# Performance work log

Hardware: AMD Instinct MI355X
Metric: run time of the kernel (lower is better)

## Reference

```python
import jax, jax.numpy as jnp
import numpy as np

def setup_inputs() -> dict:
    key = jax.random.key(0)
    k1, k2, k3 = jax.random.split(key, 3)
    B, N, D = 4, 2048, 1024
    x = jax.random.normal(k1, (B, N, D), dtype=jnp.float32)
    # nn.Linear weights are (out_features, in_features); init scale ~1/sqrt(D)
    W_Q = jax.random.normal(k2, (D, D), dtype=jnp.float32) / np.sqrt(D)
    W_K = jax.random.normal(k3, (D, D), dtype=jnp.float32) / np.sqrt(D)
    return {"x": x, "W_Q": W_Q, "W_K": W_K, "n_iters": 5}

def reference(x, W_Q, W_K, n_iters):
    # K = Linear(W_K)(x) = x @ W_K.T  -> (B, N, D)
    K = jnp.einsum('bnd,kd->bnk', x, W_K)
    y = x
    for _ in range(n_iters):
        Q = jnp.einsum('bnd,kd->bnk', y, W_Q)          # (B, N, D)
        scores = jnp.einsum('bnd,bmd->bnm', K, Q)       # K @ Q^T, (B, N, N)
        probs = jax.nn.softmax(scores, axis=-1)
        y = jnp.einsum('bnm,bmd->bnd', probs, x)        # (B, N, D)
    return y
```

## Files before the change

### kernel.cpp

```cpp
#include <hip/hip_runtime.h>
#include <cstdint>

typedef _Float16 f16;
typedef __attribute__((ext_vector_type(8))) _Float16 v8h;
typedef __attribute__((ext_vector_type(4))) float v4f;

#define LO_SCALE 4096.0f
#define LO_INV   2.44140625e-4f

__device__ __forceinline__ void split2(float f, f16& h, f16& l) {
    h = (f16)f;
    l = (f16)((f - (float)h) * LO_SCALE);
}

__device__ __forceinline__ void gload_lds16(const void* g, void* l) {
    __builtin_amdgcn_global_load_lds(
        (const __attribute__((address_space(1))) unsigned int*)(uintptr_t)g,
        (__attribute__((address_space(3))) unsigned int*)(unsigned int)(uintptr_t)l,
        16, 0, 0);
}

__global__ __launch_bounds__(256)
void gemm_nt_2limb(const f16* __restrict__ A1, const f16* __restrict__ A2,
                   const f16* __restrict__ B1, const f16* __restrict__ B2,
                   float* __restrict__ C32, f16* __restrict__ Ch,
                   f16* __restrict__ Cl, int mode, int N, int K)
{
    __shared__ f16 lds[4 * 128 * 32];
    f16* lA1 = lds;
    f16* lA2 = lds + 128 * 32;
    f16* lB1 = lds + 2 * 128 * 32;
    f16* lB2 = lds + 3 * 128 * 32;

    const int tid  = threadIdx.x;
    const int lane = tid & 63;
    const int wave = tid >> 6;
    const int wm = wave >> 1, wn = wave & 1;
    const int fr = lane & 15, quad = lane >> 4;
    const int row0 = blockIdx.y * 128;
    const int col0 = blockIdx.x * 128;
    const int l4 = lane >> 2;
    const int c8 = (lane & 3) * 8;

    v4f accB[4][4], accS[4][4];
#pragma unroll
    for (int i = 0; i < 4; ++i)
#pragma unroll
        for (int j = 0; j < 4; ++j) {
            accB[i][j] = {0.f, 0.f, 0.f, 0.f};
            accS[i][j] = {0.f, 0.f, 0.f, 0.f};
        }

    for (int k0 = 0; k0 < K; k0 += 32) {
#pragma unroll
        for (int t = 0; t < 2; ++t) {
            const int slot = wave + 4 * t;
            const int r = slot * 16 + l4;
            const size_t ga = (size_t)(row0 + r) * K + (k0 + c8);
            const size_t gb = (size_t)(col0 + r) * K + (k0 + c8);
            const unsigned loff = slot * 1024;
            gload_lds16(A1 + ga, (char*)lA1 + loff);
            gload_lds16(A2 + ga, (char*)lA2 + loff);
            gload_lds16(B1 + gb, (char*)lB1 + loff);
            gload_lds16(B2 + gb, (char*)lB2 + loff);
        }
        __syncthreads();

        v8h a1[4], a2[4], b1[4], b2[4];
#pragma unroll
        for (int i = 0; i < 4; ++i) {
            const int off = (wm * 64 + i * 16 + fr) * 32 + quad * 8;
            a1[i] = *(const v8h*)&lA1[off];
            a2[i] = *(const v8h*)&lA2[off];
        }
#pragma unroll
        for (int j = 0; j < 4; ++j) {
            const int off = (wn * 64 + j * 16 + fr) * 32 + quad * 8;
            b1[j] = *(const v8h*)&lB1[off];
            b2[j] = *(const v8h*)&lB2[off];
        }
#pragma unroll
        for (int i = 0; i < 4; ++i)
#pragma unroll
            for (int j = 0; j < 4; ++j) {
                accB[i][j] = __builtin_amdgcn_mfma_f32_16x16x32_f16(a1[i], b1[j], accB[i][j], 0, 0, 0);
                accS[i][j] = __builtin_amdgcn_mfma_f32_16x16x32_f16(a2[i], b1[j], accS[i][j], 0, 0, 0);
                accS[i][j] = __builtin_amdgcn_mfma_f32_16x16x32_f16(a1[i], b2[j], accS[i][j], 0, 0, 0);
            }
        __syncthreads();
    }

#pragma unroll
    for (int i = 0; i < 4; ++i)
#pragma unroll
        for (int j = 0; j < 4; ++j) {
            const int row = row0 + wm * 64 + i * 16 + quad * 4;
            const int col = col0 + wn * 64 + j * 16 + fr;
#pragma unroll
            for (int r = 0; r < 4; ++r) {
                const float v = accB[i][j][r] + accS[i][j][r] * LO_INV;
                const size_t off = (size_t)(row + r) * N + col;
                if (mode == 0) {
                    C32[off] = v;
                } else if (mode == 1) {
                    f16 h, l; split2(v, h, l);
                    Ch[off] = h; Cl[off] = l;
                } else {
                    C32[off] = v;
                    Ch[off] = (f16)v;
                }
            }
        }
}

__global__ __launch_bounds__(512)
void gemm_nt_2limb_256(const f16* __restrict__ A1, const f16* __restrict__ A2,
                       const f16* __restrict__ B1, const f16* __restrict__ B2,
                       float* __restrict__ C32, f16* __restrict__ Ch,
                       int N, int K)
{
    __shared__ f16 lds[2 * 24576];

    const int bid = blockIdx.x;
    const int lid = (bid & 7) * 32 + (bid >> 3);
    const int col0 = (lid & 7) * 128;
    const int row0 = (lid >> 3) * 256;

    const int tid  = threadIdx.x;
    const int lane = tid & 63;
    const int wave = tid >> 6;
    const int wm = wave >> 1;
    const int wn = wave & 1;
    const int fr = lane & 15, quad = lane >> 4;
    const int NT = K >> 5;

    const int trow = tid >> 2;
    const int tchunk = tid & 3;

    auto STAGE = [&](int T) {
        const unsigned bufB = (unsigned)(T & 1) * 49152u;
        const int k0 = T * 32;
#pragma unroll
        for (int rd = 0; rd < 2; ++rd) {
            const int r = trow + rd * 128;
            const int sc = (tchunk ^ ((r >> 1) & 3)) * 8;
            const size_t ga = (size_t)(row0 + r) * K + k0 + sc;
            const unsigned dof = (unsigned)(rd * 8192 + wave * 1024);
            gload_lds16(A1 + ga, (char*)lds + bufB + dof);
            gload_lds16(A2 + ga, (char*)lds + bufB + 16384u + dof);
        }
        {
            const int r = trow;
            const int sc = (tchunk ^ ((r >> 1) & 3)) * 8;
            const size_t gb = (size_t)(col0 + r) * K + k0 + sc;
            const unsigned dof = (unsigned)(wave * 1024);
            gload_lds16(B1 + gb, (char*)lds + bufB + 32768u + dof);
            gload_lds16(B2 + gb, (char*)lds + bufB + 40960u + dof);
        }
    };

    auto LRD = [&](const f16* base, int row) {
        return *(const v8h*)&base[row * 32 + ((quad ^ ((row >> 1) & 3)) * 8)];
    };

    v4f accB[4][4], accS[4][4];
#pragma unroll
    for (int i = 0; i < 4; ++i)
#pragma unroll
        for (int j = 0; j < 4; ++j) {
            accB[i][j] = {0.f, 0.f, 0.f, 0.f};
            accS[i][j] = {0.f, 0.f, 0.f, 0.f};
        }

    STAGE(0);
    asm volatile("s_waitcnt vmcnt(0)" ::: "memory");
    __builtin_amdgcn_s_barrier();

    for (int t = 0; t < NT; ++t) {
        const int bc = (t & 1) * 24576;
        const f16* lA1 = lds + bc;
        const f16* lA2 = lds + bc + 8192;
        const f16* lB1 = lds + bc + 16384;
        const f16* lB2 = lds + bc + 20480;

        v8h b1[4], b2[4];
#pragma unroll
        for (int j = 0; j < 4; ++j) {
            b1[j] = LRD(lB1, wn * 64 + j * 16 + fr);
            b2[j] = LRD(lB2, wn * 64 + j * 16 + fr);
        }
        {
            v8h a1 = LRD(lA1, wm * 64 + 0 + fr);
            v8h a2 = LRD(lA2, wm * 64 + 0 + fr);
            if (t + 1 < NT) STAGE(t + 1);
            __builtin_amdgcn_s_barrier();
            asm volatile("s_waitcnt lgkmcnt(0)" ::: "memory");
            __builtin_amdgcn_s_setprio(1);
#pragma unroll
            for (int j = 0; j < 4; ++j) {
                accB[0][j] = __builtin_amdgcn_mfma_f32_16x16x32_f16(a1, b1[j], accB[0][j], 0, 0, 0);
                accS[0][j] = __builtin_amdgcn_mfma_f32_16x16x32_f16(a2, b1[j], accS[0][j], 0, 0, 0);
                accS[0][j] = __builtin_amdgcn_mfma_f32_16x16x32_f16(a1, b2[j], accS[0][j], 0, 0, 0);
            }
            __builtin_amdgcn_s_setprio(0);
            __builtin_amdgcn_s_barrier();
        }

#pragma unroll
        for (int p = 1; p < 4; ++p) {
            v8h a1 = LRD(lA1, wm * 64 + p * 16 + fr);
            v8h a2 = LRD(lA2, wm * 64 + p * 16 + fr);
            __builtin_amdgcn_s_barrier();
            asm volatile("s_waitcnt lgkmcnt(0)" ::: "memory");
            __builtin_amdgcn_s_setprio(1);
#pragma unroll
            for (int j = 0; j < 4; ++j) {
                accB[p][j] = __builtin_amdgcn_mfma_f32_16x16x32_f16(a1, b1[j], accB[p][j], 0, 0, 0);
                accS[p][j] = __builtin_amdgcn_mfma_f32_16x16x32_f16(a2, b1[j], accS[p][j], 0, 0, 0);
                accS[p][j] = __builtin_amdgcn_mfma_f32_16x16x32_f16(a1, b2[j], accS[p][j], 0, 0, 0);
            }
            __builtin_amdgcn_s_setprio(0);
            if (p == 3)
                asm volatile("s_waitcnt vmcnt(0)" ::: "memory");
            __builtin_amdgcn_s_barrier();
        }
    }

#pragma unroll
    for (int i = 0; i < 4; ++i)
#pragma unroll
        for (int j = 0; j < 4; ++j) {
            const int row = row0 + wm * 64 + i * 16 + quad * 4;
            const int col = col0 + wn * 64 + j * 16 + fr;
#pragma unroll
            for (int r = 0; r < 4; ++r) {
                const float v = accB[i][j][r] + accS[i][j][r] * LO_INV;
                const size_t off = (size_t)(row + r) * N + col;
                C32[off] = v;
                Ch[off] = (f16)v;
            }
        }
}

__global__ __launch_bounds__(512)
void gemm_nt_f16_256(const f16* __restrict__ A, const f16* __restrict__ B,
                     f16* __restrict__ C, int N, int K,
                     size_t sA, size_t sB, size_t sC)
{
    __shared__ f16 lds[2 * 2 * 256 * 64];

    const int bz = blockIdx.z;
    A += (size_t)bz * sA; B += (size_t)bz * sB; C += (size_t)bz * sC;

    const int tid  = threadIdx.x;
    const int lane = tid & 63;
    const int wave = tid >> 6;
    const int wm = wave >> 2;
    const int wn = wave & 3;
    const int fr = lane & 15, quad = lane >> 4;
    const int row0 = blockIdx.y * 256;
    const int col0 = blockIdx.x * 256;
    const int NT = K >> 6;

    const int rsub = tid >> 3;
    const int csub = (((tid & 7) ^ ((tid >> 3) & 7)) * 8);

    auto STAGE = [&](int T) {
        const unsigned bufB = (unsigned)(T & 1) * 65536u;
#pragma unroll
        for (int q = 0; q < 4; ++q) {
            const f16* op = (q >= 2) ? B : A;
            const int r0 = ((q >= 2) ? col0 : row0) + (q & 1) * 128;
#pragma unroll
            for (int t2 = 0; t2 < 2; ++t2) {
                const f16* g = op + (size_t)(r0 + t2 * 64 + rsub) * K + T * 64 + csub;
                gload_lds16(g, (char*)lds + bufB + (unsigned)(q >> 1) * 32768u
                                 + (unsigned)(q & 1) * 16384u
                                 + (unsigned)(t2 * 8192 + wave * 1024));
            }
        }
    };

    auto LRD = [&](const f16* base, int row, int ks) {
        return *(const v8h*)&base[row * 64 + (((ks * 4 + quad) ^ (row & 7)) * 8)];
    };

    v4f acc[8][4];
#pragma unroll
    for (int i = 0; i < 8; ++i)
#pragma unroll
        for (int j = 0; j < 4; ++j)
            acc[i][j] = {0.f, 0.f, 0.f, 0.f};

    STAGE(0);
    asm volatile("s_waitcnt vmcnt(0)" ::: "memory");
    __builtin_amdgcn_s_barrier();

    for (int t = 0; t < NT; ++t) {
        const int bc = (t & 1) * 32768;
        const f16* lA = lds + bc;
        const f16* lB = lds + bc + 16384;

        v8h bfr[4][2];
#pragma unroll
        for (int j = 0; j < 4; ++j)
#pragma unroll
            for (int ks = 0; ks < 2; ++ks)
                bfr[j][ks] = LRD(lB, wn * 64 + j * 16 + fr, ks);
        {
            v8h a0[2], a1[2];
#pragma unroll
            for (int ks = 0; ks < 2; ++ks) {
                a0[ks] = LRD(lA, wm * 128 + 0 + fr, ks);
                a1[ks] = LRD(lA, wm * 128 + 16 + fr, ks);
            }
            if (t + 1 < NT) STAGE(t + 1);
            __builtin_amdgcn_s_barrier();
            asm volatile("s_waitcnt lgkmcnt(0)" ::: "memory");
            __builtin_amdgcn_s_setprio(1);
#pragma unroll
            for (int j = 0; j < 4; ++j) {
                acc[0][j] = __builtin_amdgcn_mfma_f32_16x16x32_f16(a0[0], bfr[j][0], acc[0][j], 0, 0, 0);
                acc[0][j] = __builtin_amdgcn_mfma_f32_16x16x32_f16(a0[1], bfr[j][1], acc[0][j], 0, 0, 0);
                acc[1][j] = __builtin_amdgcn_mfma_f32_16x16x32_f16(a1[0], bfr[j][0], acc[1][j], 0, 0, 0);
                acc[1][j] = __builtin_amdgcn_mfma_f32_16x16x32_f16(a1[1], bfr[j][1], acc[1][j], 0, 0, 0);
            }
            __builtin_amdgcn_s_setprio(0);
            __builtin_amdgcn_s_barrier();
        }

#pragma unroll
        for (int p = 1; p < 4; ++p) {
            v8h ap[2][2];
#pragma unroll
            for (int u = 0; u < 2; ++u)
#pragma unroll
                for (int ks = 0; ks < 2; ++ks)
                    ap[u][ks] = LRD(lA, wm * 128 + (p * 2 + u) * 16 + fr, ks);
            __builtin_amdgcn_s_barrier();
            asm volatile("s_waitcnt lgkmcnt(0)" ::: "memory");
            __builtin_amdgcn_s_setprio(1);
#pragma unroll
            for (int u = 0; u < 2; ++u)
#pragma unroll
                for (int j = 0; j < 4; ++j) {
                    acc[p * 2 + u][j] = __builtin_amdgcn_mfma_f32_16x16x32_f16(ap[u][0], bfr[j][0], acc[p * 2 + u][j], 0, 0, 0);
                    acc[p * 2 + u][j] = __builtin_amdgcn_mfma_f32_16x16x32_f16(ap[u][1], bfr[j][1], acc[p * 2 + u][j], 0, 0, 0);
                }
            __builtin_amdgcn_s_setprio(0);
            if (p == 3)
                asm volatile("s_waitcnt vmcnt(0)" ::: "memory");
            __builtin_amdgcn_s_barrier();
        }
    }

#pragma unroll
    for (int i = 0; i < 8; ++i)
#pragma unroll
        for (int j = 0; j < 4; ++j) {
            const int row = row0 + wm * 128 + i * 16 + quad * 4;
            const int col = col0 + wn * 64 + j * 16 + fr;
#pragma unroll
            for (int r = 0; r < 4; ++r)
                C[(size_t)(row + r) * N + col] = (f16)acc[i][j][r];
        }
}

__global__ __launch_bounds__(256)
void split_f32(const float* __restrict__ in, f16* __restrict__ h,
               f16* __restrict__ l, int n)
{
    const int i = (blockIdx.x * 256 + threadIdx.x) * 4;
    if (i >= n) return;
    const float4 v = *(const float4*)(in + i);
    f16 hh[4], ll[4];
    split2(v.x, hh[0], ll[0]);
    split2(v.y, hh[1], ll[1]);
    split2(v.z, hh[2], ll[2]);
    split2(v.w, hh[3], ll[3]);
    *(ushort4*)(h + i) = *(const ushort4*)hh;
    *(ushort4*)(l + i) = *(const ushort4*)ll;
}

__global__ __launch_bounds__(256)
void transpose_split(const float* __restrict__ in, f16* __restrict__ oh,
                     f16* __restrict__ ol, int R, int C)
{
    __shared__ float tile[32][33];
    const int tx = threadIdx.x & 31, ty = threadIdx.x >> 5;
    const int ic = blockIdx.x * 32 + tx;
    const int ir = blockIdx.y * 32 + ty;
#pragma unroll
    for (int k = 0; k < 32; k += 8)
        tile[ty + k][tx] = in[(size_t)(ir + k) * C + ic];
    __syncthreads();
    const int oc  = blockIdx.y * 32 + tx;
    const int orr = blockIdx.x * 32 + ty;
#pragma unroll
    for (int k = 0; k < 32; k += 8) {
        f16 h, l;
        split2(tile[tx][ty + k], h, l);
        oh[(size_t)(orr + k) * R + oc] = h;
        ol[(size_t)(orr + k) * R + oc] = l;
    }
}

#define CAP 1024

__global__ __launch_bounds__(256)
void refine_pv(const f16* __restrict__ S, const float* __restrict__ Kt,
               const float* __restrict__ Y, const float* __restrict__ X,
               float* __restrict__ Yout, f16* __restrict__ Yh)
{
    const int r = blockIdx.x;
    const int b = r >> 11;
    const int t = threadIdx.x;
    const int wave = t >> 6, lane = t & 63;

    __shared__ float red[4];
    __shared__ float wmax[4], wsum[4];
    __shared__ int cnt;
    __shared__ int idxs[CAP];
    __shared__ float accL[4][1024];

    const float* krow = Kt + (size_t)r * 1024;
    float4 kf[4];
#pragma unroll
    for (int d = 0; d < 4; ++d)
        kf[d] = *(const float4*)(krow + d * 256 + lane * 4);

    float s[8];
    {
        const v8h sv = *(const v8h*)(S + (size_t)r * 2048 + t * 8);
#pragma unroll
        for (int k = 0; k < 8; ++k) s[k] = (float)sv[k];
    }
    float m = s[0];
#pragma unroll
    for (int k = 1; k < 8; ++k) m = fmaxf(m, s[k]);
#pragma unroll
    for (int off = 32; off > 0; off >>= 1) m = fmaxf(m, __shfl_xor(m, off));
    if (lane == 0) red[wave] = m;
    if (t == 0) cnt = 0;
    __syncthreads();
    m = fmaxf(fmaxf(red[0], red[1]), fmaxf(red[2], red[3]));

    const float thresh = m - 18.0f;
#pragma unroll
    for (int k = 0; k < 8; ++k)
        if (s[k] > thresh) {
            const int p = atomicAdd(&cnt, 1);
            if (p < CAP) idxs[p] = t * 8 + k;
        }
    __syncthreads();
    const int count = min(cnt, CAP);

    const float* ybase = Y + ((size_t)b << 21);
    const float* xbase = X + ((size_t)b << 21);
    float m_run = m;
    float sum = 0.f;
    float4 acc[4];
#pragma unroll
    for (int d = 0; d < 4; ++d) acc[d] = {0.f, 0.f, 0.f, 0.f};

    for (int j = wave; j < count; j += 4) {
        const int idx = idxs[j];
        const float* yrow = ybase + (size_t)idx * 1024;
        float e = 0.f;
#pragma unroll
        for (int d = 0; d < 4; ++d) {
            const float4 yv = *(const float4*)(yrow + d * 256 + lane * 4);
            e += kf[d].x * yv.x + kf[d].y * yv.y + kf[d].z * yv.z + kf[d].w * yv.w;
        }
#pragma unroll
        for (int off = 32; off > 0; off >>= 1) e += __shfl_xor(e, off);
        if (e > m_run) {
            const float sc = expf(m_run - e);
            sum *= sc;
#pragma unroll
            for (int d = 0; d < 4; ++d) {
                acc[d].x *= sc; acc[d].y *= sc; acc[d].z *= sc; acc[d].w *= sc;
            }
            m_run = e;
        }
        const float w = expf(e - m_run);
        sum += w;
        const float* xrow = xbase + (size_t)idx * 1024;
#pragma unroll
        for (int d = 0; d < 4; ++d) {
            const float4 xv = *(const float4*)(xrow + d * 256 + lane * 4);
            acc[d].x += w * xv.x; acc[d].y += w * xv.y;
            acc[d].z += w * xv.z; acc[d].w += w * xv.w;
        }
    }

    if (lane == 0) { wmax[wave] = m_run; wsum[wave] = sum; }
    __syncthreads();
    const float M = fmaxf(fmaxf(wmax[0], wmax[1]), fmaxf(wmax[2], wmax[3]));
    float Stot = 0.f;
#pragma unroll
    for (int v = 0; v < 4; ++v) Stot += wsum[v] * expf(wmax[v] - M);
    const float scale = expf(m_run - M) / Stot;
#pragma unroll
    for (int d = 0; d < 4; ++d) {
        const int e0 = d * 256 + lane * 4;
        float4 a = acc[d];
        a.x *= scale; a.y *= scale; a.z *= scale; a.w *= scale;
        *(float4*)&accL[wave][e0] = a;
    }
    __syncthreads();

    const int e0 = t * 4;
    float4 o = *(const float4*)&accL[0][e0];
    const float4 o1 = *(const float4*)&accL[1][e0];
    const float4 o2 = *(const float4*)&accL[2][e0];
    const float4 o3 = *(const float4*)&accL[3][e0];
    o.x += o1.x + o2.x + o3.x;
    o.y += o1.y + o2.y + o3.y;
    o.z += o1.z + o2.z + o3.z;
    o.w += o1.w + o2.w + o3.w;

    const size_t oo = (size_t)r * 1024 + e0;
    *(float4*)(Yout + oo) = o;
    f16 h[4] = {(f16)o.x, (f16)o.y, (f16)o.z, (f16)o.w};
    *(ushort4*)(Yh + oo) = *(const ushort4*)h;
}

extern "C" void kernel_launch(void* const* d_in, const int* in_sizes, int n_in,
                              void* d_out, int out_size, void* d_ws, size_t ws_size,
                              hipStream_t stream)
{
    const float* x  = (const float*)d_in[0];
    const float* Wq = (const float*)d_in[1];
    const float* Wk = (const float*)d_in[2];
    const int n_iters = 5;

    const size_t NXe = 8388608;
    const size_t NWe = 1048576;
    const size_t NSe = 16777216;
    const size_t NR  = 8192;

    char* p = (char*)d_ws;
    f16* xh   = (f16*)p; p += NXe * 2;
    f16* xl   = (f16*)p; p += NXe * 2;
    f16* wkth = (f16*)p; p += NWe * 2;
    f16* wktl = (f16*)p; p += NWe * 2;
    f16* wqth = (f16*)p; p += NWe * 2;
    f16* wqtl = (f16*)p; p += NWe * 2;
    f16* vth  = (f16*)p; p += NWe * 2;
    f16* vtl  = (f16*)p; p += NWe * 2;
    float* kt32 = (float*)p; p += NXe * 4;
    f16*  kt16  = (f16*)p;  p += NXe * 2;
    f16*  st    = (f16*)p;  p += NSe * 2;
    f16*  yh    = (f16*)p;  p += NXe * 2;
    float* y1   = (float*)p; p += NXe * 4;
    float* y2   = (float*)p; p += NXe * 4;
    if ((size_t)(p - (char*)d_ws) > ws_size) return;

    float* out = (float*)d_out;

    split_f32<<<dim3(NXe / 1024), dim3(256), 0, stream>>>(x, xh, xl, (int)NXe);
    transpose_split<<<dim3(32, 32), dim3(256), 0, stream>>>(Wk, wkth, wktl, 1024, 1024);
    transpose_split<<<dim3(32, 32), dim3(256), 0, stream>>>(Wq, wqth, wqtl, 1024, 1024);
    gemm_nt_2limb<<<dim3(8, 8), dim3(256), 0, stream>>>(
        wqth, wqtl, wkth, wktl, nullptr, vth, vtl, 1, 1024, 1024);
    gemm_nt_2limb_256<<<dim3(256), dim3(512), 0, stream>>>(
        xh, xl, vth, vtl, kt32, kt16, 1024, 1024);

    const float* yr = x;
    float* pingpong[2] = {y1, y2};
    for (int it = 0; it < n_iters; ++it) {
        float* yw = (it == n_iters - 1) ? out : pingpong[it & 1];
        const f16* Bop = (it == 0) ? xh : yh;
        gemm_nt_f16_256<<<dim3(8, 8, 4), dim3(512), 0, stream>>>(
            kt16, Bop, st, 2048, 1024,
            (size_t)2048 * 1024, (size_t)2048 * 1024, (size_t)2048 * 2048);
        refine_pv<<<dim3(NR), dim3(256), 0, stream>>>(
            st, kt32, yr, x, yw, yh);
        yr = yw;
    }
}
```

Before: 716.4 us.

## Run refine_pv with one wavefront per row and prefetch Y/X rows together

Shrinks the per-row refinement kernel from four wavefronts to a single 64-lane wavefront that scans all candidate indices itself. This removes the block-wide barriers, the cross-wave max/sum merge and the 16KB LDS reduction buffer, so occupancy can rise. The Y and X rows for each candidate are now loaded together up front to expose more memory-level parallelism. The cost is that each row's candidate loop runs serially in one wave, which lengthens rows that have many candidates.

New measurement: 784.3 us. +9.5%, slower.

```diff
diff --git a/kernel.cpp b/kernel.cpp
--- a/kernel.cpp
+++ b/kernel.cpp
@@ -407,21 +407,17 @@
 
 #define CAP 1024
 
-__global__ __launch_bounds__(256)
+__global__ __launch_bounds__(64)
 void refine_pv(const f16* __restrict__ S, const float* __restrict__ Kt,
                const float* __restrict__ Y, const float* __restrict__ X,
                float* __restrict__ Yout, f16* __restrict__ Yh)
 {
     const int r = blockIdx.x;
     const int b = r >> 11;
-    const int t = threadIdx.x;
-    const int wave = t >> 6, lane = t & 63;
-
-    __shared__ float red[4];
-    __shared__ float wmax[4], wsum[4];
-    __shared__ int cnt;
+    const int lane = threadIdx.x;
+
     __shared__ int idxs[CAP];
-    __shared__ float accL[4][1024];
+    __shared__ int cnt_s;
 
     const float* krow = Kt + (size_t)r * 1024;
     float4 kf[4];
@@ -429,31 +425,33 @@
     for (int d = 0; d < 4; ++d)
         kf[d] = *(const float4*)(krow + d * 256 + lane * 4);
 
-    float s[8];
-    {
-        const v8h sv = *(const v8h*)(S + (size_t)r * 2048 + t * 8);
-#pragma unroll
-        for (int k = 0; k < 8; ++k) s[k] = (float)sv[k];
-    }
-    float m = s[0];
-#pragma unroll
-    for (int k = 1; k < 8; ++k) m = fmaxf(m, s[k]);
+    const f16* srow = S + (size_t)r * 2048;
+    v8h sv[4];
+#pragma unroll
+    for (int c = 0; c < 4; ++c)
+        sv[c] = *(const v8h*)(srow + c * 512 + lane * 8);
+
+    if (lane == 0) cnt_s = 0;
+
+    float m = -3.0e38f;
+#pragma unroll
+    for (int c = 0; c < 4; ++c)
+#pragma unroll
+        for (int k = 0; k < 8; ++k)
+            m = fmaxf(m, (float)sv[c][k]);
 #pragma unroll
     for (int off = 32; off > 0; off >>= 1) m = fmaxf(m, __shfl_xor(m, off));
-    if (lane == 0) red[wave] = m;
-    if (t == 0) cnt = 0;
-    __syncthreads();
-    m = fmaxf(fmaxf(red[0], red[1]), fmaxf(red[2], red[3]));
 
     const float thresh = m - 18.0f;
 #pragma unroll
-    for (int k = 0; k < 8; ++k)
-        if (s[k] > thresh) {
-            const int p = atomicAdd(&cnt, 1);
-            if (p < CAP) idxs[p] = t * 8 + k;
-        }
-    __syncthreads();
-    const int count = min(cnt, CAP);
+    for (int c = 0; c < 4; ++c)
+#pragma unroll
+        for (int k = 0; k < 8; ++k)
+            if ((float)sv[c][k] > thresh) {
+                const int p = atomicAdd(&cnt_s, 1);
+                if (p < CAP) idxs[p] = c * 512 + lane * 8 + k;
+            }
+    const int count = min(cnt_s, CAP);
 
     const float* ybase = Y + ((size_t)b << 21);
     const float* xbase = X + ((size_t)b << 21);
@@ -463,15 +461,21 @@
 #pragma unroll
     for (int d = 0; d < 4; ++d) acc[d] = {0.f, 0.f, 0.f, 0.f};
 
-    for (int j = wave; j < count; j += 4) {
+    for (int j = 0; j < count; ++j) {
         const int idx = idxs[j];
         const float* yrow = ybase + (size_t)idx * 1024;
+        const float* xrow = xbase + (size_t)idx * 1024;
+        float4 yv[4], xv[4];
+#pragma unroll
+        for (int d = 0; d < 4; ++d) {
+            yv[d] = *(const float4*)(yrow + d * 256 + lane * 4);
+            xv[d] = *(const float4*)(xrow + d * 256 + lane * 4);
+        }
         float e = 0.f;
 #pragma unroll
-        for (int d = 0; d < 4; ++d) {
-            const float4 yv = *(const float4*)(yrow + d * 256 + lane * 4);
-            e += kf[d].x * yv.x + kf[d].y * yv.y + kf[d].z * yv.z + kf[d].w * yv.w;
-        }
+        for (int d = 0; d < 4; ++d)
+            e += kf[d].x * yv[d].x + kf[d].y * yv[d].y
+               + kf[d].z * yv[d].z + kf[d].w * yv[d].w;
 #pragma unroll
         for (int off = 32; off > 0; off >>= 1) e += __shfl_xor(e, off);
         if (e > m_run) {
@@ -485,45 +489,23 @@
         }
         const float w = expf(e - m_run);
         sum += w;
-        const float* xrow = xbase + (size_t)idx * 1024;
 #pragma unroll
         for (int d = 0; d < 4; ++d) {
-            const float4 xv = *(const float4*)(xrow + d * 256 + lane * 4);
-            acc[d].x += w * xv.x; acc[d].y += w * xv.y;
-            acc[d].z += w * xv.z; acc[d].w += w * xv.w;
-        }
-    }
-
-    if (lane == 0) { wmax[wave] = m_run; wsum[wave] = sum; }
-    __syncthreads();
-    const float M = fmaxf(fmaxf(wmax[0], wmax[1]), fmaxf(wmax[2], wmax[3]));
-    float Stot = 0.f;
-#pragma unroll
-    for (int v = 0; v < 4; ++v) Stot += wsum[v] * expf(wmax[v] - M);
-    const float scale = expf(m_run - M) / Stot;
+            acc[d].x += w * xv[d].x; acc[d].y += w * xv[d].y;
+            acc[d].z += w * xv[d].z; acc[d].w += w * xv[d].w;
+        }
+    }
+
+    const float inv = 1.0f / sum;
 #pragma unroll
     for (int d = 0; d < 4; ++d) {
-        const int e0 = d * 256 + lane * 4;
-        float4 a = acc[d];
-        a.x *= scale; a.y *= scale; a.z *= scale; a.w *= scale;
-        *(float4*)&accL[wave][e0] = a;
-    }
-    __syncthreads();
-
-    const int e0 = t * 4;
-    float4 o = *(const float4*)&accL[0][e0];
-    const float4 o1 = *(const float4*)&accL[1][e0];
-    const float4 o2 = *(const float4*)&accL[2][e0];
-    const float4 o3 = *(const float4*)&accL[3][e0];
-    o.x += o1.x + o2.x + o3.x;
-    o.y += o1.y + o2.y + o3.y;
-    o.z += o1.z + o2.z + o3.z;
-    o.w += o1.w + o2.w + o3.w;
-
-    const size_t oo = (size_t)r * 1024 + e0;
-    *(float4*)(Yout + oo) = o;
-    f16 h[4] = {(f16)o.x, (f16)o.y, (f16)o.z, (f16)o.w};
-    *(ushort4*)(Yh + oo) = *(const ushort4*)h;
+        float4 o = acc[d];
+        o.x *= inv; o.y *= inv; o.z *= inv; o.w *= inv;
+        const size_t oo = (size_t)r * 1024 + d * 256 + lane * 4;
+        *(float4*)(Yout + oo) = o;
+        f16 h[4] = {(f16)o.x, (f16)o.y, (f16)o.z, (f16)o.w};
+        *(ushort4*)(Yh + oo) = *(const ushort4*)h;
+    }
 }
 
 extern "C" void kernel_launch(void* const* d_in, const int* in_sizes, int n_in,
@@ -575,7 +557,7 @@
         gemm_nt_f16_256<<<dim3(8, 8, 4), dim3(512), 0, stream>>>(
             kt16, Bop, st, 2048, 1024,
             (size_t)2048 * 1024, (size_t)2048 * 1024, (size_t)2048 * 2048);
-        refine_pv<<<dim3(NR), dim3(256), 0, stream>>>(
+        refine_pv<<<dim3(NR), dim3(64), 0, stream>>>(
             st, kt32, yr, x, yw, yh);
         yr = yw;
     }
```

## Fuse row-max and candidate selection into score GEMM epilogue, drop score matrix

Applied to the files above, without the earlier changes.

The score GEMM no longer writes the full B×N×N fp16 score matrix. Its epilogue computes per-tile row maxima (merged globally with atomicMax on order-preserving uint keys) and appends each score within 18 of the tile-local max, with its column, to a per-row candidate list. refine_pv then filters that list against the global row max instead of reading and scanning a 2048-wide score row, which removes a large write and read of scores each iteration. In exchange it adds global atomics and two memsets per iteration, and rows with more than 512 candidates are silently truncated.

Measured after the change: 911.2 us. 1.27x slower.

```diff
diff --git a/kernel.cpp b/kernel.cpp
--- a/kernel.cpp
+++ b/kernel.cpp
@@ -18,6 +18,15 @@
         (const __attribute__((address_space(1))) unsigned int*)(uintptr_t)g,
         (__attribute__((address_space(3))) unsigned int*)(unsigned int)(uintptr_t)l,
         16, 0, 0);
+}
+
+__device__ __forceinline__ unsigned mapf(float f) {
+    unsigned b = __float_as_uint(f);
+    return b ^ (unsigned)(((int)b >> 31) | 0x80000000);
+}
+__device__ __forceinline__ float unmapf(unsigned u) {
+    unsigned b = u ^ ((u & 0x80000000u) ? 0x80000000u : 0xFFFFFFFFu);
+    return __uint_as_float(b);
 }
 
 __global__ __launch_bounds__(256)
@@ -242,15 +251,19 @@
         }
 }
 
+#define LCAP 512
+
 __global__ __launch_bounds__(512)
-void gemm_nt_f16_256(const f16* __restrict__ A, const f16* __restrict__ B,
-                     f16* __restrict__ C, int N, int K,
-                     size_t sA, size_t sB, size_t sC)
+void gemm_sel(const f16* __restrict__ A, const f16* __restrict__ B,
+              uint2* __restrict__ list, int* __restrict__ cntG,
+              unsigned* __restrict__ rowMaxG, int K,
+              size_t sA, size_t sB)
 {
     __shared__ f16 lds[2 * 2 * 256 * 64];
+    __shared__ unsigned rowmaxL[256];
 
     const int bz = blockIdx.z;
-    A += (size_t)bz * sA; B += (size_t)bz * sB; C += (size_t)bz * sC;
+    A += (size_t)bz * sA; B += (size_t)bz * sB;
 
     const int tid  = threadIdx.x;
     const int lane = tid & 63;
@@ -354,15 +367,45 @@
         }
     }
 
+    if (tid < 256) rowmaxL[tid] = 0u;
+    __syncthreads();
+
 #pragma unroll
     for (int i = 0; i < 8; ++i)
 #pragma unroll
-        for (int j = 0; j < 4; ++j) {
-            const int row = row0 + wm * 128 + i * 16 + quad * 4;
-            const int col = col0 + wn * 64 + j * 16 + fr;
-#pragma unroll
-            for (int r = 0; r < 4; ++r)
-                C[(size_t)(row + r) * N + col] = (f16)acc[i][j][r];
+        for (int rr = 0; rr < 4; ++rr) {
+            float mloc = fmaxf(fmaxf(acc[i][0][rr], acc[i][1][rr]),
+                               fmaxf(acc[i][2][rr], acc[i][3][rr]));
+#pragma unroll
+            for (int off = 1; off < 16; off <<= 1)
+                mloc = fmaxf(mloc, __shfl_xor(mloc, off));
+            if (fr == 0)
+                atomicMax(&rowmaxL[wm * 128 + i * 16 + quad * 4 + rr], mapf(mloc));
+        }
+    __syncthreads();
+
+    const int rbase = bz * 2048 + row0;
+    if (tid < 256)
+        atomicMax(&rowMaxG[rbase + tid], rowmaxL[tid]);
+
+#pragma unroll
+    for (int i = 0; i < 8; ++i)
+#pragma unroll
+        for (int rr = 0; rr < 4; ++rr) {
+            const int lrow = wm * 128 + i * 16 + quad * 4 + rr;
+            const float th = unmapf(rowmaxL[lrow]) - 18.0f;
+#pragma unroll
+            for (int j = 0; j < 4; ++j) {
+                const float s = acc[i][j][rr];
+                if (s > th) {
+                    const int grow = rbase + lrow;
+                    const int p = atomicAdd(&cntG[grow], 1);
+                    if (p < LCAP)
+                        list[(size_t)grow * LCAP + p] =
+                            make_uint2(__float_as_uint(s),
+                                       (unsigned)(col0 + wn * 64 + j * 16 + fr));
+                }
+            }
         }
 }
 
@@ -405,10 +448,10 @@
     }
 }
 
-#define CAP 1024
-
 __global__ __launch_bounds__(256)
-void refine_pv(const f16* __restrict__ S, const float* __restrict__ Kt,
+void refine_pv(const uint2* __restrict__ list, const int* __restrict__ cntG,
+               const unsigned* __restrict__ rowMaxG,
+               const float* __restrict__ Kt,
                const float* __restrict__ Y, const float* __restrict__ X,
                float* __restrict__ Yout, f16* __restrict__ Yh)
 {
@@ -417,10 +460,9 @@
     const int t = threadIdx.x;
     const int wave = t >> 6, lane = t & 63;
 
-    __shared__ float red[4];
     __shared__ float wmax[4], wsum[4];
     __shared__ int cnt;
-    __shared__ int idxs[CAP];
+    __shared__ int idxs[LCAP];
     __shared__ float accL[4][1024];
 
     const float* krow = Kt + (size_t)r * 1024;
@@ -429,35 +471,24 @@
     for (int d = 0; d < 4; ++d)
         kf[d] = *(const float4*)(krow + d * 256 + lane * 4);
 
-    float s[8];
-    {
-        const v8h sv = *(const v8h*)(S + (size_t)r * 2048 + t * 8);
-#pragma unroll
-        for (int k = 0; k < 8; ++k) s[k] = (float)sv[k];
-    }
-    float m = s[0];
-#pragma unroll
-    for (int k = 1; k < 8; ++k) m = fmaxf(m, s[k]);
-#pragma unroll
-    for (int off = 32; off > 0; off >>= 1) m = fmaxf(m, __shfl_xor(m, off));
-    if (lane == 0) red[wave] = m;
+    const float M0 = unmapf(rowMaxG[r]);
+    const float thresh = M0 - 18.0f;
     if (t == 0) cnt = 0;
     __syncthreads();
-    m = fmaxf(fmaxf(red[0], red[1]), fmaxf(red[2], red[3]));
-
-    const float thresh = m - 18.0f;
-#pragma unroll
-    for (int k = 0; k < 8; ++k)
-        if (s[k] > thresh) {
+    const int cg = min(cntG[r], LCAP);
+    for (int j = t; j < cg; j += 256) {
+        const uint2 e = list[(size_t)r * LCAP + j];
+        if (__uint_as_float(e.x) > thresh) {
             const int p = atomicAdd(&cnt, 1);
-            if (p < CAP) idxs[p] = t * 8 + k;
-        }
+            idxs[p] = (int)e.y;
+        }
+    }
     __syncthreads();
-    const int count = min(cnt, CAP);
+    const int count = cnt;
 
     const float* ybase = Y + ((size_t)b << 21);
     const float* xbase = X + ((size_t)b << 21);
-    float m_run = m;
+    float m_run = M0;
     float sum = 0.f;
     float4 acc[4];
 #pragma unroll
@@ -537,7 +568,6 @@
 
     const size_t NXe = 8388608;
     const size_t NWe = 1048576;
-    const size_t NSe = 16777216;
     const size_t NR  = 8192;
 
     char* p = (char*)d_ws;
@@ -551,7 +581,9 @@
     f16* vtl  = (f16*)p; p += NWe * 2;
     float* kt32 = (float*)p; p += NXe * 4;
     f16*  kt16  = (f16*)p;  p += NXe * 2;
-    f16*  st    = (f16*)p;  p += NSe * 2;
+    uint2* list = (uint2*)p; p += NR * LCAP * 8;
+    int* cntG = (int*)p; p += NR * 4;
+    unsigned* rowMaxG = (unsigned*)p; p += NR * 4;
     f16*  yh    = (f16*)p;  p += NXe * 2;
     float* y1   = (float*)p; p += NXe * 4;
     float* y2   = (float*)p; p += NXe * 4;
@@ -572,11 +604,13 @@
     for (int it = 0; it < n_iters; ++it) {
         float* yw = (it == n_iters - 1) ? out : pingpong[it & 1];
         const f16* Bop = (it == 0) ? xh : yh;
-        gemm_nt_f16_256<<<dim3(8, 8, 4), dim3(512), 0, stream>>>(
-            kt16, Bop, st, 2048, 1024,
-            (size_t)2048 * 1024, (size_t)2048 * 1024, (size_t)2048 * 2048);
-        refine_pv<<<dim3(NR), dim3(256), 0, stream>>>(
-            st, kt32, yr, x, yw, yh);
+        hipMemsetAsync(cntG, 0, NR * 4, stream);
+        hipMemsetAsync(rowMaxG, 0, NR * 4, stream);
+        gemm_sel<<<dim3(8, 8, 4), dim3(512), 0, stream>>>(
+            kt16, Bop, list, cntG, rowMaxG, 1024,
+            (size_t)2048 * 1024, (size_t)2048 * 1024);
+        refine_pv<<<dim3((unsigned)NR), dim3(256), 0, stream>>>(
+            list, cntG, rowMaxG, kt32, yr, x, yw, yh);
         yr = yw;
     }
 }
```

## Make refine_pv persistent with atomic row queue and double-buffered row loads

Applied to the files above, without the earlier changes.

The refine_pv kernel becomes persistent: 2048 blocks, each tied to one of 8 chunks, take rows dynamically through a global atomic counter instead of one block per row. This balances the uneven per-row work that comes from the data-dependent candidate count. The inner loop also prefetches the next candidate's Y and X rows into registers while the current one is computed, to hide global load latency. This adds a memset of the counters, an atomic per row, and higher register pressure from the prefetch buffers.

Result: slower. 1.044 ms (+45.8%).

```diff
diff --git a/kernel.cpp b/kernel.cpp
--- a/kernel.cpp
+++ b/kernel.cpp
@@ -410,120 +410,157 @@
 __global__ __launch_bounds__(256)
 void refine_pv(const f16* __restrict__ S, const float* __restrict__ Kt,
                const float* __restrict__ Y, const float* __restrict__ X,
-               float* __restrict__ Yout, f16* __restrict__ Yh)
+               float* __restrict__ Yout, f16* __restrict__ Yh,
+               int* __restrict__ ctr)
 {
-    const int r = blockIdx.x;
-    const int b = r >> 11;
+    const int chunk = blockIdx.x & 7;
     const int t = threadIdx.x;
     const int wave = t >> 6, lane = t & 63;
 
     __shared__ float red[4];
     __shared__ float wmax[4], wsum[4];
     __shared__ int cnt;
+    __shared__ int rowS;
     __shared__ int idxs[CAP];
     __shared__ float accL[4][1024];
 
-    const float* krow = Kt + (size_t)r * 1024;
-    float4 kf[4];
-#pragma unroll
-    for (int d = 0; d < 4; ++d)
-        kf[d] = *(const float4*)(krow + d * 256 + lane * 4);
-
-    float s[8];
-    {
-        const v8h sv = *(const v8h*)(S + (size_t)r * 2048 + t * 8);
-#pragma unroll
-        for (int k = 0; k < 8; ++k) s[k] = (float)sv[k];
+    for (;;) {
+        if (t == 0) rowS = atomicAdd(&ctr[chunk], 1);
+        __syncthreads();
+        const int rs = rowS;
+        if (rs >= 1024) break;
+        const int r = (chunk << 10) | rs;
+        const int b = r >> 11;
+
+        const float* krow = Kt + (size_t)r * 1024;
+        float4 kf[4];
+#pragma unroll
+        for (int d = 0; d < 4; ++d)
+            kf[d] = *(const float4*)(krow + d * 256 + lane * 4);
+
+        float s[8];
+        {
+            const v8h sv = *(const v8h*)(S + (size_t)r * 2048 + t * 8);
+#pragma unroll
+            for (int k = 0; k < 8; ++k) s[k] = (float)sv[k];
+        }
+        float m = s[0];
+#pragma unroll
+        for (int k = 1; k < 8; ++k) m = fmaxf(m, s[k]);
+#pragma unroll
+        for (int off = 32; off > 0; off >>= 1) m = fmaxf(m, __shfl_xor(m, off));
+        if (lane == 0) red[wave] = m;
+        if (t == 0) cnt = 0;
+        __syncthreads();
+        m = fmaxf(fmaxf(red[0], red[1]), fmaxf(red[2], red[3]));
+
+        const float thresh = m - 18.0f;
+#pragma unroll
+        for (int k = 0; k < 8; ++k)
+            if (s[k] > thresh) {
+                const int p = atomicAdd(&cnt, 1);
+                if (p < CAP) idxs[p] = t * 8 + k;
+            }
+        __syncthreads();
+        const int count = min(cnt, CAP);
+
+        const float* ybase = Y + ((size_t)b << 21);
+        const float* xbase = X + ((size_t)b << 21);
+        float m_run = m;
+        float sum = 0.f;
+        float4 acc[4];
+#pragma unroll
+        for (int d = 0; d < 4; ++d) acc[d] = {0.f, 0.f, 0.f, 0.f};
+
+        int j = wave;
+        if (j < count) {
+            float4 yv0[4], xv0[4];
+            {
+                const int idx = idxs[j];
+                const float* yrow = ybase + (size_t)idx * 1024;
+                const float* xrow = xbase + (size_t)idx * 1024;
+#pragma unroll
+                for (int d = 0; d < 4; ++d) {
+                    yv0[d] = *(const float4*)(yrow + d * 256 + lane * 4);
+                    xv0[d] = *(const float4*)(xrow + d * 256 + lane * 4);
+                }
+            }
+            for (;;) {
+                const int jn = j + 4;
+                const bool more = jn < count;
+                float4 yv1[4], xv1[4];
+                if (more) {
+                    const int idx1 = idxs[jn];
+                    const float* yrow = ybase + (size_t)idx1 * 1024;
+                    const float* xrow = xbase + (size_t)idx1 * 1024;
+#pragma unroll
+                    for (int d = 0; d < 4; ++d) {
+                        yv1[d] = *(const float4*)(yrow + d * 256 + lane * 4);
+                        xv1[d] = *(const float4*)(xrow + d * 256 + lane * 4);
+                    }
+                }
+                float e = 0.f;
+#pragma unroll
+                for (int d = 0; d < 4; ++d)
+                    e += kf[d].x * yv0[d].x + kf[d].y * yv0[d].y
+                       + kf[d].z * yv0[d].z + kf[d].w * yv0[d].w;
+#pragma unroll
+                for (int off = 32; off > 0; off >>= 1) e += __shfl_xor(e, off);
+                if (e > m_run) {
+                    const float sc = expf(m_run - e);
+                    sum *= sc;
+#pragma unroll
+                    for (int d = 0; d < 4; ++d) {
+                        acc[d].x *= sc; acc[d].y *= sc;
+                        acc[d].z *= sc; acc[d].w *= sc;
+                    }
+                    m_run = e;
+                }
+                const float w = expf(e - m_run);
+                sum += w;
+#pragma unroll
+                for (int d = 0; d < 4; ++d) {
+                    acc[d].x += w * xv0[d].x; acc[d].y += w * xv0[d].y;
+                    acc[d].z += w * xv0[d].z; acc[d].w += w * xv0[d].w;
+                }
+                if (!more) break;
+                j = jn;
+#pragma unroll
+                for (int d = 0; d < 4; ++d) { yv0[d] = yv1[d]; xv0[d] = xv1[d]; }
+            }
+        }
+
+        if (lane == 0) { wmax[wave] = m_run; wsum[wave] = sum; }
+        __syncthreads();
+        const float M = fmaxf(fmaxf(wmax[0], wmax[1]), fmaxf(wmax[2], wmax[3]));
+        float Stot = 0.f;
+#pragma unroll
+        for (int v = 0; v < 4; ++v) Stot += wsum[v] * expf(wmax[v] - M);
+        const float scale = expf(m_run - M) / Stot;
+#pragma unroll
+        for (int d = 0; d < 4; ++d) {
+            const int e0 = d * 256 + lane * 4;
+            float4 a = acc[d];
+            a.x *= scale; a.y *= scale; a.z *= scale; a.w *= scale;
+            *(float4*)&accL[wave][e0] = a;
+        }
+        __syncthreads();
+
+        const int e0 = t * 4;
+        float4 o = *(const float4*)&accL[0][e0];
+        const float4 o1 = *(const float4*)&accL[1][e0];
+        const float4 o2 = *(const float4*)&accL[2][e0];
+        const float4 o3 = *(const float4*)&accL[3][e0];
+        o.x += o1.x + o2.x + o3.x;
+        o.y += o1.y + o2.y + o3.y;
+        o.z += o1.z + o2.z + o3.z;
+        o.w += o1.w + o2.w + o3.w;
+
+        const size_t oo = (size_t)r * 1024 + e0;
+        *(float4*)(Yout + oo) = o;
+        f16 h[4] = {(f16)o.x, (f16)o.y, (f16)o.z, (f16)o.w};
+        *(ushort4*)(Yh + oo) = *(const ushort4*)h;
     }
-    float m = s[0];
-#pragma unroll
-    for (int k = 1; k < 8; ++k) m = fmaxf(m, s[k]);
-#pragma unroll
-    for (int off = 32; off > 0; off >>= 1) m = fmaxf(m, __shfl_xor(m, off));
-    if (lane == 0) red[wave] = m;
-    if (t == 0) cnt = 0;
-    __syncthreads();
-    m = fmaxf(fmaxf(red[0], red[1]), fmaxf(red[2], red[3]));
-
-    const float thresh = m - 18.0f;
-#pragma unroll
-    for (int k = 0; k < 8; ++k)
-        if (s[k] > thresh) {
-            const int p = atomicAdd(&cnt, 1);
-            if (p < CAP) idxs[p] = t * 8 + k;
-        }
-    __syncthreads();
-    const int count = min(cnt, CAP);
-
-    const float* ybase = Y + ((size_t)b << 21);
-    const float* xbase = X + ((size_t)b << 21);
-    float m_run = m;
-    float sum = 0.f;
-    float4 acc[4];
-#pragma unroll
-    for (int d = 0; d < 4; ++d) acc[d] = {0.f, 0.f, 0.f, 0.f};
-
-    for (int j = wave; j < count; j += 4) {
-        const int idx = idxs[j];
-        const float* yrow = ybase + (size_t)idx * 1024;
-        float e = 0.f;
-#pragma unroll
-        for (int d = 0; d < 4; ++d) {
-            const float4 yv = *(const float4*)(yrow + d * 256 + lane * 4);
-            e += kf[d].x * yv.x + kf[d].y * yv.y + kf[d].z * yv.z + kf[d].w * yv.w;
-        }
-#pragma unroll
-        for (int off = 32; off > 0; off >>= 1) e += __shfl_xor(e, off);
-        if (e > m_run) {
-            const float sc = expf(m_run - e);
-            sum *= sc;
-#pragma unroll
-            for (int d = 0; d < 4; ++d) {
-                acc[d].x *= sc; acc[d].y *= sc; acc[d].z *= sc; acc[d].w *= sc;
-            }
-            m_run = e;
-        }
-        const float w = expf(e - m_run);
-        sum += w;
-        const float* xrow = xbase + (size_t)idx * 1024;
-#pragma unroll
-        for (int d = 0; d < 4; ++d) {
-            const float4 xv = *(const float4*)(xrow + d * 256 + lane * 4);
-            acc[d].x += w * xv.x; acc[d].y += w * xv.y;
-            acc[d].z += w * xv.z; acc[d].w += w * xv.w;
-        }
-    }
-
-    if (lane == 0) { wmax[wave] = m_run; wsum[wave] = sum; }
-    __syncthreads();
-    const float M = fmaxf(fmaxf(wmax[0], wmax[1]), fmaxf(wmax[2], wmax[3]));
-    float Stot = 0.f;
-#pragma unroll
-    for (int v = 0; v < 4; ++v) Stot += wsum[v] * expf(wmax[v] - M);
-    const float scale = expf(m_run - M) / Stot;
-#pragma unroll
-    for (int d = 0; d < 4; ++d) {
-        const int e0 = d * 256 + lane * 4;
-        float4 a = acc[d];
-        a.x *= scale; a.y *= scale; a.z *= scale; a.w *= scale;
-        *(float4*)&accL[wave][e0] = a;
-    }
-    __syncthreads();
-
-    const int e0 = t * 4;
-    float4 o = *(const float4*)&accL[0][e0];
-    const float4 o1 = *(const float4*)&accL[1][e0];
-    const float4 o2 = *(const float4*)&accL[2][e0];
-    const float4 o3 = *(const float4*)&accL[3][e0];
-    o.x += o1.x + o2.x + o3.x;
-    o.y += o1.y + o2.y + o3.y;
-    o.z += o1.z + o2.z + o3.z;
-    o.w += o1.w + o2.w + o3.w;
-
-    const size_t oo = (size_t)r * 1024 + e0;
-    *(float4*)(Yout + oo) = o;
-    f16 h[4] = {(f16)o.x, (f16)o.y, (f16)o.z, (f16)o.w};
-    *(ushort4*)(Yh + oo) = *(const ushort4*)h;
 }
 
 extern "C" void kernel_launch(void* const* d_in, const int* in_sizes, int n_in,
@@ -538,7 +575,6 @@
     const size_t NXe = 8388608;
     const size_t NWe = 1048576;
     const size_t NSe = 16777216;
-    const size_t NR  = 8192;
 
     char* p = (char*)d_ws;
     f16* xh   = (f16*)p; p += NXe * 2;
@@ -555,10 +591,12 @@
     f16*  yh    = (f16*)p;  p += NXe * 2;
     float* y1   = (float*)p; p += NXe * 4;
     float* y2   = (float*)p; p += NXe * 4;
+    int* ctr    = (int*)p;   p += 256;
     if ((size_t)(p - (char*)d_ws) > ws_size) return;
 
     float* out = (float*)d_out;
 
+    hipMemsetAsync(ctr, 0, 5 * 8 * sizeof(int), stream);
     split_f32<<<dim3(NXe / 1024), dim3(256), 0, stream>>>(x, xh, xl, (int)NXe);
     transpose_split<<<dim3(32, 32), dim3(256), 0, stream>>>(Wk, wkth, wktl, 1024, 1024);
     transpose_split<<<dim3(32, 32), dim3(256), 0, stream>>>(Wq, wqth, wqtl, 1024, 1024);
@@ -575,8 +613,8 @@
         gemm_nt_f16_256<<<dim3(8, 8, 4), dim3(512), 0, stream>>>(
             kt16, Bop, st, 2048, 1024,
             (size_t)2048 * 1024, (size_t)2048 * 1024, (size_t)2048 * 2048);
-        refine_pv<<<dim3(NR), dim3(256), 0, stream>>>(
-            st, kt32, yr, x, yw, yh);
+        refine_pv<<<dim3(2048), dim3(256), 0, stream>>>(
+            st, kt32, yr, x, yw, yh, ctr + it * 8);
         yr = yw;
     }
 }
```
